# Optimization experiments

Hardware: AMD Instinct MI355X
Metric: run time of the kernel (lower is better)

Reference implementation:

```python
import jax, jax.numpy as jnp
import numpy as np

DIM = 256
N = 262144
LN_EPS = 1e-5


def setup_inputs() -> dict:
    key = jax.random.key(0)
    ks = jax.random.split(key, 16)
    d = DIM
    inp = {
        "x": jax.random.normal(ks[0], (N, d), dtype=jnp.float32),
        # main cell params (torch Linear stores weight as [out, in])
        "W_slow": jax.random.normal(ks[1], (d, d), dtype=jnp.float32) / np.sqrt(d),
        "V_slow": jax.random.normal(ks[2], (d, d), dtype=jnp.float32) * (0.1 / np.sqrt(d)),
        "gate_w": jax.random.normal(ks[3], (1, d), dtype=jnp.float32) / np.sqrt(d),
        "gate_b": jnp.zeros((1,), dtype=jnp.float32),
        # homeostatic core: Linear(4,16) -> LN(16) -> Tanh -> Linear(16,8) -> ReLU -> Linear(8,4) -> Sigmoid
        "sens1_w": jax.random.normal(ks[4], (16, 4), dtype=jnp.float32) * 0.5,
        "sens1_b": jnp.zeros((16,), dtype=jnp.float32),
        "ln_g": jnp.ones((16,), dtype=jnp.float32),
        "ln_b": jnp.zeros((16,), dtype=jnp.float32),
        "sens2_w": jax.random.normal(ks[5], (8, 16), dtype=jnp.float32) * 0.25,
        "sens2_b": jnp.zeros((8,), dtype=jnp.float32),
        "act_w": jax.random.normal(ks[6], (4, 8), dtype=jnp.float32) * 0.35,
        "act_b": jnp.zeros((4,), dtype=jnp.float32),
        # persistent Hebbian memory buffer
        "semantic_memory": jax.random.normal(ks[7], (d, d), dtype=jnp.float32) * 0.01,
    }
    return inp


def _homeostatic_controls(x, h_raw, w_norm, sens1_w, sens1_b, ln_g, ln_b,
                          sens2_w, sens2_b, act_w, act_b):
    # state vector: [surprise, excitation, fatigue, coherence]  -> [N, 4]
    surprise = jnp.abs(jnp.var(x, axis=1) - 0.5)          # unbiased=False variance
    excitation = jnp.mean(jnp.abs(h_raw), axis=1)
    fatigue = jnp.full_like(surprise, w_norm)
    coherence = jnp.full_like(surprise, 0.5)              # loss_val is None
    state = jnp.stack([surprise, excitation, fatigue, coherence], axis=1)
    z = state @ sens1_w.T + sens1_b                        # [N,16]
    mu = jnp.mean(z, axis=-1, keepdims=True)
    var = jnp.mean((z - mu) ** 2, axis=-1, keepdims=True)
    z = (z - mu) * jax.lax.rsqrt(var + LN_EPS) * ln_g + ln_b
    z = jnp.tanh(z)
    z = jax.nn.relu(z @ sens2_w.T + sens2_b)               # [N,8]
    controls = jax.nn.sigmoid(z @ act_w.T + act_b)         # [N,4]
    return controls


def reference(x, W_slow, V_slow, gate_w, gate_b,
              sens1_w, sens1_b, ln_g, ln_b, sens2_w, sens2_b, act_w, act_b,
              semantic_memory):
    # v = clamp(V_slow(x), -2, 2)
    v = jnp.clip(x @ V_slow.T, -2.0, 2.0)                  # [N, d]

    # homeostatic core (no_grad in torch)
    h_raw = x @ W_slow.T
    w_norm = jnp.linalg.norm(W_slow)
    controls = _homeostatic_controls(x, h_raw, w_norm, sens1_w, sens1_b,
                                     ln_g, ln_b, sens2_w, sens2_b, act_w, act_b)
    metabolic_rate = jnp.mean(controls[:, 0])
    gate_value = jnp.mean(controls[:, 2])

    gate = jax.nn.sigmoid(v @ gate_w.T + gate_b) * gate_value  # [N,1]
    output = jnp.clip(gate * v, -2.0, 2.0)

    # training-mode Hebbian memory update (no_grad in torch)
    batch = x.shape[0]
    hebb = (v.T @ x) / batch                               # [d, d]
    forget = jnp.mean(v ** 2, axis=0)[:, None] * semantic_memory
    delta = jnp.tanh(hebb - forget)
    mem = semantic_memory + delta * metabolic_rate * 0.1
    mem_norm = jnp.maximum(jnp.linalg.norm(mem), 1e-6)
    new_memory = mem / mem_norm * 0.5

    return output, new_memory
```

## Files before the change

kernel.cpp:

```cpp
#include <hip/hip_runtime.h>
#include <hip/hip_bf16.h>


#define NTOK 262144

typedef short s16x4 __attribute__((ext_vector_type(4)));
typedef short s16x8 __attribute__((ext_vector_type(8)));
typedef float f32x4 __attribute__((ext_vector_type(4)));
typedef unsigned int u32x4 __attribute__((ext_vector_type(4)));
typedef __bf16 bf16x8 __attribute__((ext_vector_type(8)));

static __device__ __forceinline__ float b2f(short s) {
  unsigned int u = ((unsigned int)(unsigned short)s) << 16;
  return __builtin_bit_cast(float, u);
}
static __device__ __forceinline__ short f2b(float f) {
  __hip_bfloat16 h = __float2bfloat16(f);
  return (short)__builtin_bit_cast(unsigned short, h);
}
static __device__ __forceinline__ float clip2(float f) {
  return fminf(2.f, fmaxf(-2.f, f));
}
static __device__ __forceinline__ unsigned int packu(short lo, short hi) {
  return (unsigned int)(unsigned short)lo | ((unsigned int)(unsigned short)hi << 16);
}
static __device__ __forceinline__ f32x4 mfma16(s16x8 a, s16x8 b, f32x4 c) {
  return __builtin_amdgcn_mfma_f32_16x16x32_bf16(
      __builtin_bit_cast(bf16x8, a), __builtin_bit_cast(bf16x8, b), c, 0, 0, 0);
}

__global__ __launch_bounds__(1024) void k_prep(const float* __restrict__ V,
                                               const float* __restrict__ W,
                                               short* __restrict__ Vb,
                                               short* __restrict__ Wb,
                                               float* __restrict__ scal) {
  int t = blockIdx.x * 1024 + threadIdx.x;
  f32x4 v4 = *(const f32x4*)(V + (size_t)t * 4);
  f32x4 w4 = *(const f32x4*)(W + (size_t)t * 4);
  s16x4 vb, wb;
  float s = 0.f;
#pragma unroll
  for (int e = 0; e < 4; ++e) {
    vb[e] = f2b(v4[e]);
    wb[e] = f2b(w4[e]);
    s += w4[e] * w4[e];
  }
  *(s16x4*)(Vb + (size_t)t * 4) = vb;
  *(s16x4*)(Wb + (size_t)t * 4) = wb;
#pragma unroll
  for (int d = 1; d < 64; d <<= 1) s += __shfl_xor(s, d);
  __shared__ float r[16];
  if ((threadIdx.x & 63) == 0) r[threadIdx.x >> 6] = s;
  __syncthreads();
  if (threadIdx.x == 0) {
    float tt = 0.f;
#pragma unroll
    for (int i = 0; i < 16; ++i) tt += r[i];
    atomicAdd(&scal[0], tt);
  }
}

__global__ __launch_bounds__(512) void k_main(
    const float* __restrict__ x, const short* __restrict__ Vb,
    const short* __restrict__ Wb, const float* __restrict__ gw,
    const float* __restrict__ gb, const float* __restrict__ s1w,
    const float* __restrict__ s1b, const float* __restrict__ lng,
    const float* __restrict__ lnb, const float* __restrict__ s2w,
    const float* __restrict__ s2b, const float* __restrict__ aw,
    const float* __restrict__ ab, short* __restrict__ v_out,
    float* __restrict__ g_out, float* __restrict__ scal) {
  __shared__ __align__(16) short xs[64 * 40];
  __shared__ float red[256];
  int tid = threadIdx.x;
  int lane = tid & 63, wid = tid >> 6;
  int lr = lane & 15, lg = lane >> 4;
  int mat = wid >> 2, wc = wid & 3;
  size_t r0 = (size_t)blockIdx.x * 64;

  f32x4 acc[4][4] = {};
  float sx = 0.f, sxx = 0.f;
  int srow = tid >> 3, skc = tid & 7;

  const short* Bm = mat ? Wb : Vb;
  const short* bbase = Bm + (size_t)(wc * 64 + lr) * 256 + lg * 8;
  const float* xsrc = x + (r0 + srow) * 256 + skc * 4;

  f32x4 rx = *(const f32x4*)(xsrc);
  s16x8 bcur[4], bnext[4];
#pragma unroll
  for (int nf = 0; nf < 4; ++nf)
    bcur[nf] = *(const s16x8*)(bbase + nf * 16 * 256);

#pragma unroll
  for (int ks = 0; ks < 8; ++ks) {
    {
      s16x4 c;
#pragma unroll
      for (int e = 0; e < 4; ++e) {
        float f = rx[e];
        sx += f;
        sxx += f * f;
        c[e] = f2b(f);
      }
      *(s16x4*)(xs + srow * 40 + skc * 4) = c;
    }
    __syncthreads();
    if (ks < 7) {
      rx = *(const f32x4*)(xsrc + (ks + 1) * 32);
#pragma unroll
      for (int nf = 0; nf < 4; ++nf)
        bnext[nf] = *(const s16x8*)(bbase + nf * 16 * 256 + (ks + 1) * 32);
    }
#pragma unroll
    for (int mf = 0; mf < 4; ++mf) {
      s16x8 a = *(const s16x8*)(xs + (mf * 16 + lr) * 40 + lg * 8);
#pragma unroll
      for (int nf = 0; nf < 4; ++nf)
        acc[mf][nf] = mfma16(a, bcur[nf], acc[mf][nf]);
    }
    __syncthreads();
#pragma unroll
    for (int nf = 0; nf < 4; ++nf) bcur[nf] = bnext[nf];
  }

  float pl[4][4];
  if (mat == 0) {
    float gw4[4];
#pragma unroll
    for (int nf = 0; nf < 4; ++nf) gw4[nf] = gw[wc * 64 + nf * 16 + lr];
#pragma unroll
    for (int mf = 0; mf < 4; ++mf)
#pragma unroll
      for (int e = 0; e < 4; ++e) {
        float g = 0.f;
#pragma unroll
        for (int nf = 0; nf < 4; ++nf) {
          float v = clip2(acc[mf][nf][e]);
          acc[mf][nf][e] = v;
          g += v * gw4[nf];
        }
        pl[mf][e] = g;
      }
  } else {
#pragma unroll
    for (int mf = 0; mf < 4; ++mf)
#pragma unroll
      for (int e = 0; e < 4; ++e) {
        float hbs = 0.f;
#pragma unroll
        for (int nf = 0; nf < 4; ++nf) hbs += fabsf(acc[mf][nf][e]);
        pl[mf][e] = hbs;
      }
  }
#pragma unroll
  for (int d = 1; d < 16; d <<= 1)
#pragma unroll
    for (int mf = 0; mf < 4; ++mf)
#pragma unroll
      for (int e = 0; e < 4; ++e) pl[mf][e] += __shfl_xor(pl[mf][e], d);
  sx += __shfl_xor(sx, 1); sx += __shfl_xor(sx, 2); sx += __shfl_xor(sx, 4);
  sxx += __shfl_xor(sxx, 1); sxx += __shfl_xor(sxx, 2); sxx += __shfl_xor(sxx, 4);

  if (tid < 128) red[tid] = 0.f;
  __syncthreads();
  if (lr == 0) {
#pragma unroll
    for (int mf = 0; mf < 4; ++mf)
#pragma unroll
      for (int e = 0; e < 4; ++e) {
        int row = mf * 16 + lg * 4 + e;
        atomicAdd(&red[mat * 64 + row], pl[mf][e]);
      }
  }
  if ((tid & 7) == 0) { red[128 + srow] = sx; red[192 + srow] = sxx; }
  if (mat == 0) {
#pragma unroll
    for (int mf = 0; mf < 4; ++mf)
#pragma unroll
      for (int nf = 0; nf < 4; ++nf)
#pragma unroll
        for (int e = 0; e < 4; ++e) {
          int row = mf * 16 + lg * 4 + e;
          int col = wc * 64 + nf * 16 + lr;
          v_out[(r0 + row) * 256 + col] = f2b(acc[mf][nf][e]);
        }
  }
  __syncthreads();

  float c0v = 0.f, c2v = 0.f;
  if (tid < 64) {
    int row = tid;
    float mean = red[128 + row] * (1.f / 256.f);
    float var = red[192 + row] * (1.f / 256.f) - mean * mean;
    float st[4];
    st[0] = fabsf(var - 0.5f);
    st[1] = red[64 + row] * (1.f / 256.f);
    st[2] = sqrtf(scal[0]);
    st[3] = 0.5f;
    float z[16];
#pragma unroll
    for (int o = 0; o < 16; ++o) {
      float a = s1b[o];
#pragma unroll
      for (int i = 0; i < 4; ++i) a += s1w[o * 4 + i] * st[i];
      z[o] = a;
    }
    float mu = 0.f;
#pragma unroll
    for (int o = 0; o < 16; ++o) mu += z[o];
    mu *= (1.f / 16.f);
    float vz = 0.f;
#pragma unroll
    for (int o = 0; o < 16; ++o) { float d2 = z[o] - mu; vz += d2 * d2; }
    vz *= (1.f / 16.f);
    float rs = rsqrtf(vz + 1e-5f);
#pragma unroll
    for (int o = 0; o < 16; ++o)
      z[o] = tanhf((z[o] - mu) * rs * lng[o] + lnb[o]);
    float z2[8];
#pragma unroll
    for (int o = 0; o < 8; ++o) {
      float a = s2b[o];
#pragma unroll
      for (int i = 0; i < 16; ++i) a += s2w[o * 16 + i] * z[i];
      z2[o] = fmaxf(a, 0.f);
    }
    float cc[2];
#pragma unroll
    for (int q = 0; q < 2; ++q) {
      int o = q * 2;
      float a = ab[o];
#pragma unroll
      for (int i = 0; i < 8; ++i) a += aw[o * 8 + i] * z2[i];
      cc[q] = 1.f / (1.f + expf(-a));
    }
    c0v = cc[0]; c2v = cc[1];
    float graw = red[row] + gb[0];
    g_out[r0 + row] = 1.f / (1.f + expf(-graw));
  }
#pragma unroll
  for (int d = 1; d < 64; d <<= 1) {
    c0v += __shfl_xor(c0v, d);
    c2v += __shfl_xor(c2v, d);
  }
  if (tid == 0) {
    atomicAdd(&scal[1], c0v);
    atomicAdd(&scal[2], c2v);
  }
}

__global__ __launch_bounds__(512, 2) void k_hebb(
    const float* __restrict__ x, const short* __restrict__ v_in,
    const float* __restrict__ g_sig, const float* __restrict__ scal,
    float* __restrict__ colv2, float* __restrict__ parts,
    float* __restrict__ out0) {
  __shared__ __align__(16) unsigned int ldsT[2 * 256 * 17];
  unsigned int* vT = ldsT;
  unsigned int* xT = ldsT + 256 * 17;
  int tid = threadIdx.x;
  int lane = tid & 63, wid = tid >> 6;
  int lr = lane & 15, lg = lane >> 4;
  int wr = wid >> 2, wc = wid & 3;
  size_t n0 = (size_t)blockIdx.x * 1024;
  float gv = scal[2] * (1.f / 262144.f);

  f32x4 acc[8][4] = {};
  float cv2[8] = {0.f, 0.f, 0.f, 0.f, 0.f, 0.f, 0.f, 0.f};
  int np = tid >> 5, ic = tid & 31, i0 = ic * 8;

  for (int nt = 0; nt < 32; ++nt) {
    size_t nr = n0 + nt * 32 + np * 2;
    s16x8 va = *(const s16x8*)(v_in + nr * 256 + i0);
    s16x8 vb = *(const s16x8*)(v_in + (nr + 1) * 256 + i0);
    f32x4 xa0 = *(const f32x4*)(x + nr * 256 + i0);
    f32x4 xa1 = *(const f32x4*)(x + nr * 256 + i0 + 4);
    f32x4 xb0 = *(const f32x4*)(x + (nr + 1) * 256 + i0);
    f32x4 xb1 = *(const f32x4*)(x + (nr + 1) * 256 + i0 + 4);
    float sa = g_sig[nr] * gv, sb = g_sig[nr + 1] * gv;
    f32x4 oa0, oa1, ob0, ob1;
#pragma unroll
    for (int j = 0; j < 4; ++j) {
      float fa = b2f(va[j]), fA = b2f(va[4 + j]);
      float fb = b2f(vb[j]), fB = b2f(vb[4 + j]);
      cv2[j] += fa * fa + fb * fb;
      cv2[4 + j] += fA * fA + fB * fB;
      oa0[j] = clip2(fa * sa); oa1[j] = clip2(fA * sa);
      ob0[j] = clip2(fb * sb); ob1[j] = clip2(fB * sb);
      vT[(i0 + j) * 17 + np] = packu(va[j], vb[j]);
      vT[(i0 + 4 + j) * 17 + np] = packu(va[4 + j], vb[4 + j]);
      xT[(i0 + j) * 17 + np] = packu(f2b(xa0[j]), f2b(xb0[j]));
      xT[(i0 + 4 + j) * 17 + np] = packu(f2b(xa1[j]), f2b(xb1[j]));
    }
    *(f32x4*)(out0 + nr * 256 + i0) = oa0;
    *(f32x4*)(out0 + nr * 256 + i0 + 4) = oa1;
    *(f32x4*)(out0 + (nr + 1) * 256 + i0) = ob0;
    *(f32x4*)(out0 + (nr + 1) * 256 + i0 + 4) = ob1;
    __syncthreads();
    int npb = lg * 4;
    s16x8 bfr[4];
#pragma unroll
    for (int nf = 0; nf < 4; ++nf) {
      int j = wc * 64 + nf * 16 + lr;
      u32x4 q;
      q[0] = xT[j * 17 + npb]; q[1] = xT[j * 17 + npb + 1];
      q[2] = xT[j * 17 + npb + 2]; q[3] = xT[j * 17 + npb + 3];
      bfr[nf] = __builtin_bit_cast(s16x8, q);
    }
#pragma unroll
    for (int mf = 0; mf < 8; ++mf) {
      int i = wr * 128 + mf * 16 + lr;
      u32x4 q;
      q[0] = vT[i * 17 + npb]; q[1] = vT[i * 17 + npb + 1];
      q[2] = vT[i * 17 + npb + 2]; q[3] = vT[i * 17 + npb + 3];
      s16x8 afr = __builtin_bit_cast(s16x8, q);
#pragma unroll
      for (int nf = 0; nf < 4; ++nf)
        acc[mf][nf] = mfma16(afr, bfr[nf], acc[mf][nf]);
    }
    __syncthreads();
  }
  float* myp = parts + (size_t)blockIdx.x * 65536;
#pragma unroll
  for (int mf = 0; mf < 8; ++mf)
#pragma unroll
    for (int nf = 0; nf < 4; ++nf)
#pragma unroll
      for (int e = 0; e < 4; ++e) {
        int i = wr * 128 + mf * 16 + lg * 4 + e;
        int j = wc * 64 + nf * 16 + lr;
        myp[i * 256 + j] = acc[mf][nf][e];
      }
  __syncthreads();
  float* cred = (float*)ldsT;
  if (tid < 256) cred[tid] = 0.f;
  __syncthreads();
#pragma unroll
  for (int j = 0; j < 8; ++j) atomicAdd(&cred[i0 + j], cv2[j]);
  __syncthreads();
  if (tid < 256) atomicAdd(&colv2[tid], cred[tid]);
}

__global__ __launch_bounds__(256) void k_mem1(
    const float* __restrict__ parts, const float* __restrict__ colv2,
    const float* __restrict__ sm, float* __restrict__ mem,
    float* __restrict__ scal) {
  int i = blockIdx.x, j = threadIdx.x;
  float hebb = 0.f;
#pragma unroll 8
  for (int p = 0; p < 256; ++p) hebb += parts[(size_t)p * 65536 + i * 256 + j];
  hebb *= (1.f / 262144.f);
  float mr = scal[1] * (1.f / 262144.f);
  float smv = sm[i * 256 + j];
  float forget = colv2[i] * (1.f / 262144.f) * smv;
  float delta = tanhf(hebb - forget);
  float m = smv + delta * mr * 0.1f;
  mem[i * 256 + j] = m;
  float s = m * m;
#pragma unroll
  for (int d = 1; d < 64; d <<= 1) s += __shfl_xor(s, d);
  __shared__ float r4[4];
  if ((j & 63) == 0) r4[j >> 6] = s;
  __syncthreads();
  if (j == 0) atomicAdd(&scal[3], r4[0] + r4[1] + r4[2] + r4[3]);
}

__global__ __launch_bounds__(256) void k_mem2(const float* __restrict__ mem,
                                              const float* __restrict__ scal,
                                              float* __restrict__ out1) {
  int idx = blockIdx.x * 256 + threadIdx.x;
  float scale = 0.5f / fmaxf(sqrtf(scal[3]), 1e-6f);
  out1[idx] = mem[idx] * scale;
}

extern "C" void kernel_launch(void* const* d_in, const int* in_sizes, int n_in,
                              void* d_out, int out_size, void* d_ws, size_t ws_size,
                              hipStream_t stream) {
  (void)in_sizes; (void)n_in; (void)out_size; (void)ws_size;
  const float* x   = (const float*)d_in[0];
  const float* Wm  = (const float*)d_in[1];
  const float* Vm  = (const float*)d_in[2];
  const float* gw  = (const float*)d_in[3];
  const float* gb  = (const float*)d_in[4];
  const float* s1w = (const float*)d_in[5];
  const float* s1b = (const float*)d_in[6];
  const float* lng = (const float*)d_in[7];
  const float* lnb = (const float*)d_in[8];
  const float* s2w = (const float*)d_in[9];
  const float* s2b = (const float*)d_in[10];
  const float* aw  = (const float*)d_in[11];
  const float* ab  = (const float*)d_in[12];
  const float* sm  = (const float*)d_in[13];
  float* out0 = (float*)d_out;
  float* out1 = out0 + (size_t)NTOK * 256;

  char* w = (char*)d_ws;
  short* v_ws  = (short*)w;
  float* g_ws  = (float*)(w + 134217728);
  float* scal  = (float*)(w + 135266304);
  float* colv2 = (float*)(w + 135266560);
  float* mem   = (float*)(w + 135267584);
  float* parts = (float*)(w + 135529728);
  short* Vb    = (short*)(w + 202638592);
  short* Wb    = (short*)(w + 202769664);

  hipMemsetAsync(scal, 0, 1280, stream);
  k_prep<<<16, 1024, 0, stream>>>(Vm, Wm, Vb, Wb, scal);
  k_main<<<4096, 512, 0, stream>>>(x, Vb, Wb, gw, gb, s1w, s1b, lng, lnb,
                                   s2w, s2b, aw, ab, v_ws, g_ws, scal);
  k_hebb<<<256, 512, 0, stream>>>(x, v_ws, g_ws, scal, colv2, parts, out0);
  k_mem1<<<256, 256, 0, stream>>>(parts, colv2, sm, mem, scal);
  k_mem2<<<256, 256, 0, stream>>>(mem, scal, out1);
}
```

Baseline: 408.8 us.

## Process four row tiles per block with double-buffered K=64 LDS pipeline in k_main

k_main now handles 256 rows per block (four 64-row tiles) instead of 64, and launches a quarter as many blocks. The K loop moves from K=32 steps to K=64 steps. It uses a double-buffered LDS tile with x loads issued two steps ahead, which leaves a single barrier per step. This is meant to hide global-load latency and amortise per-block setup. The cost is more registers, fewer blocks in flight, and a per-tile epilogue that is serialised inside each block.

```diff
diff --git a/kernel.cpp b/kernel.cpp
--- a/kernel.cpp
+++ b/kernel.cpp
@@ -69,184 +69,217 @@
     const float* __restrict__ s2b, const float* __restrict__ aw,
     const float* __restrict__ ab, short* __restrict__ v_out,
     float* __restrict__ g_out, float* __restrict__ scal) {
-  __shared__ __align__(16) short xs[64 * 40];
+  __shared__ __align__(16) short xs[2][64 * 72];
   __shared__ float red[256];
   int tid = threadIdx.x;
   int lane = tid & 63, wid = tid >> 6;
   int lr = lane & 15, lg = lane >> 4;
   int mat = wid >> 2, wc = wid & 3;
-  size_t r0 = (size_t)blockIdx.x * 64;
+  size_t bid = blockIdx.x;
 
   f32x4 acc[4][4] = {};
-  float sx = 0.f, sxx = 0.f;
+  float sx = 0.f, sxx = 0.f, sx_t = 0.f, sxx_t = 0.f;
   int srow = tid >> 3, skc = tid & 7;
 
   const short* Bm = mat ? Wb : Vb;
   const short* bbase = Bm + (size_t)(wc * 64 + lr) * 256 + lg * 8;
-  const float* xsrc = x + (r0 + srow) * 256 + skc * 4;
-
-  f32x4 rx = *(const f32x4*)(xsrc);
-  s16x8 bcur[4], bnext[4];
-#pragma unroll
-  for (int nf = 0; nf < 4; ++nf)
-    bcur[nf] = *(const s16x8*)(bbase + nf * 16 * 256);
-
-#pragma unroll
-  for (int ks = 0; ks < 8; ++ks) {
-    {
-      s16x4 c;
-#pragma unroll
-      for (int e = 0; e < 4; ++e) {
-        float f = rx[e];
-        sx += f;
-        sxx += f * f;
-        c[e] = f2b(f);
-      }
-      *(s16x4*)(xs + srow * 40 + skc * 4) = c;
-    }
+
+  f32x4 rxa0, rxb0, rxa1, rxb1;
+
+#define XPTR(c)                                                         \
+  (x + ((size_t)bid * 256 + (size_t)((c) >> 2) * 64 + srow) * 256 +     \
+   ((c) & 3) * 64 + skc * 8)
+#define ISSUE(c, A, B_)                      \
+  {                                          \
+    int cc = (c) > 15 ? 15 : (c);            \
+    const float* p_ = XPTR(cc);              \
+    A = *(const f32x4*)p_;                   \
+    B_ = *(const f32x4*)(p_ + 4);            \
+  }
+#define CONVERT(A, B_, buf)                                   \
+  {                                                           \
+    s16x8 c8;                                                 \
+    _Pragma("unroll") for (int e = 0; e < 4; ++e) {           \
+      float f0 = A[e], f1 = B_[e];                            \
+      sx += f0 + f1;                                          \
+      sxx += f0 * f0 + f1 * f1;                               \
+      c8[e] = f2b(f0);                                        \
+      c8[4 + e] = f2b(f1);                                    \
+    }                                                         \
+    *(s16x8*)(&xs[buf][srow * 72 + skc * 8]) = c8;            \
+  }
+#define STEP(g, RAi, RBi, RAc, RBc)                                        \
+  {                                                                        \
+    ISSUE((g) + 2, RAi, RBi);                                              \
+    s16x8 bfr[4][2];                                                       \
+    _Pragma("unroll") for (int nf = 0; nf < 4; ++nf)                       \
+        _Pragma("unroll") for (int kk = 0; kk < 2; ++kk)                   \
+            bfr[nf][kk] = *(const s16x8*)(bbase + nf * 16 * 256 +          \
+                                          ((g) & 3) * 64 + kk * 32);       \
+    CONVERT(RAc, RBc, ((g) + 1) & 1);                                      \
+    _Pragma("unroll") for (int mf = 0; mf < 4; ++mf) {                     \
+      s16x8 a0 = *(const s16x8*)(&xs[(g) & 1][(mf * 16 + lr) * 72 +        \
+                                              lg * 8]);                    \
+      s16x8 a1 = *(const s16x8*)(&xs[(g) & 1][(mf * 16 + lr) * 72 + 32 +   \
+                                              lg * 8]);                    \
+      _Pragma("unroll") for (int nf = 0; nf < 4; ++nf) {                   \
+        acc[mf][nf] = mfma16(a0, bfr[nf][0], acc[mf][nf]);                 \
+        acc[mf][nf] = mfma16(a1, bfr[nf][1], acc[mf][nf]);                 \
+      }                                                                    \
+    }                                                                      \
+    __syncthreads();                                                       \
+  }
+
+  ISSUE(0, rxa0, rxb0);
+  ISSUE(1, rxa1, rxb1);
+  CONVERT(rxa0, rxb0, 0);
+  __syncthreads();
+
+  for (int t = 0; t < 4; ++t) {
+    int g0 = t * 4;
+    STEP(g0 + 0, rxa0, rxb0, rxa1, rxb1);
+    STEP(g0 + 1, rxa1, rxb1, rxa0, rxb0);
+    STEP(g0 + 2, rxa0, rxb0, rxa1, rxb1);
+    sx_t = sx; sxx_t = sxx; sx = 0.f; sxx = 0.f;
+    STEP(g0 + 3, rxa1, rxb1, rxa0, rxb0);
+
+    size_t r0 = bid * 256 + (size_t)t * 64;
+    float pl[4][4];
+    if (mat == 0) {
+      float gw4[4];
+#pragma unroll
+      for (int nf = 0; nf < 4; ++nf) gw4[nf] = gw[wc * 64 + nf * 16 + lr];
+#pragma unroll
+      for (int mf = 0; mf < 4; ++mf)
+#pragma unroll
+        for (int e = 0; e < 4; ++e) {
+          float g = 0.f;
+#pragma unroll
+          for (int nf = 0; nf < 4; ++nf) {
+            float v = clip2(acc[mf][nf][e]);
+            acc[mf][nf][e] = v;
+            g += v * gw4[nf];
+          }
+          pl[mf][e] = g;
+        }
+    } else {
+#pragma unroll
+      for (int mf = 0; mf < 4; ++mf)
+#pragma unroll
+        for (int e = 0; e < 4; ++e) {
+          float hbs = 0.f;
+#pragma unroll
+          for (int nf = 0; nf < 4; ++nf) hbs += fabsf(acc[mf][nf][e]);
+          pl[mf][e] = hbs;
+        }
+    }
+#pragma unroll
+    for (int d = 1; d < 16; d <<= 1)
+#pragma unroll
+      for (int mf = 0; mf < 4; ++mf)
+#pragma unroll
+        for (int e = 0; e < 4; ++e) pl[mf][e] += __shfl_xor(pl[mf][e], d);
+    sx_t += __shfl_xor(sx_t, 1); sx_t += __shfl_xor(sx_t, 2);
+    sx_t += __shfl_xor(sx_t, 4);
+    sxx_t += __shfl_xor(sxx_t, 1); sxx_t += __shfl_xor(sxx_t, 2);
+    sxx_t += __shfl_xor(sxx_t, 4);
+
+    if (tid < 128) red[tid] = 0.f;
     __syncthreads();
-    if (ks < 7) {
-      rx = *(const f32x4*)(xsrc + (ks + 1) * 32);
-#pragma unroll
-      for (int nf = 0; nf < 4; ++nf)
-        bnext[nf] = *(const s16x8*)(bbase + nf * 16 * 256 + (ks + 1) * 32);
-    }
-#pragma unroll
-    for (int mf = 0; mf < 4; ++mf) {
-      s16x8 a = *(const s16x8*)(xs + (mf * 16 + lr) * 40 + lg * 8);
-#pragma unroll
-      for (int nf = 0; nf < 4; ++nf)
-        acc[mf][nf] = mfma16(a, bcur[nf], acc[mf][nf]);
-    }
-    __syncthreads();
-#pragma unroll
-    for (int nf = 0; nf < 4; ++nf) bcur[nf] = bnext[nf];
-  }
-
-  float pl[4][4];
-  if (mat == 0) {
-    float gw4[4];
-#pragma unroll
-    for (int nf = 0; nf < 4; ++nf) gw4[nf] = gw[wc * 64 + nf * 16 + lr];
-#pragma unroll
-    for (int mf = 0; mf < 4; ++mf)
-#pragma unroll
-      for (int e = 0; e < 4; ++e) {
-        float g = 0.f;
-#pragma unroll
-        for (int nf = 0; nf < 4; ++nf) {
-          float v = clip2(acc[mf][nf][e]);
-          acc[mf][nf][e] = v;
-          g += v * gw4[nf];
-        }
-        pl[mf][e] = g;
-      }
-  } else {
-#pragma unroll
-    for (int mf = 0; mf < 4; ++mf)
-#pragma unroll
-      for (int e = 0; e < 4; ++e) {
-        float hbs = 0.f;
-#pragma unroll
-        for (int nf = 0; nf < 4; ++nf) hbs += fabsf(acc[mf][nf][e]);
-        pl[mf][e] = hbs;
-      }
-  }
-#pragma unroll
-  for (int d = 1; d < 16; d <<= 1)
-#pragma unroll
-    for (int mf = 0; mf < 4; ++mf)
-#pragma unroll
-      for (int e = 0; e < 4; ++e) pl[mf][e] += __shfl_xor(pl[mf][e], d);
-  sx += __shfl_xor(sx, 1); sx += __shfl_xor(sx, 2); sx += __shfl_xor(sx, 4);
-  sxx += __shfl_xor(sxx, 1); sxx += __shfl_xor(sxx, 2); sxx += __shfl_xor(sxx, 4);
-
-  if (tid < 128) red[tid] = 0.f;
-  __syncthreads();
-  if (lr == 0) {
-#pragma unroll
-    for (int mf = 0; mf < 4; ++mf)
-#pragma unroll
-      for (int e = 0; e < 4; ++e) {
-        int row = mf * 16 + lg * 4 + e;
-        atomicAdd(&red[mat * 64 + row], pl[mf][e]);
-      }
-  }
-  if ((tid & 7) == 0) { red[128 + srow] = sx; red[192 + srow] = sxx; }
-  if (mat == 0) {
-#pragma unroll
-    for (int mf = 0; mf < 4; ++mf)
-#pragma unroll
-      for (int nf = 0; nf < 4; ++nf)
+    if (lr == 0) {
+#pragma unroll
+      for (int mf = 0; mf < 4; ++mf)
 #pragma unroll
         for (int e = 0; e < 4; ++e) {
           int row = mf * 16 + lg * 4 + e;
-          int col = wc * 64 + nf * 16 + lr;
-          v_out[(r0 + row) * 256 + col] = f2b(acc[mf][nf][e]);
+          atomicAdd(&red[mat * 64 + row], pl[mf][e]);
         }
-  }
-  __syncthreads();
-
-  float c0v = 0.f, c2v = 0.f;
-  if (tid < 64) {
-    int row = tid;
-    float mean = red[128 + row] * (1.f / 256.f);
-    float var = red[192 + row] * (1.f / 256.f) - mean * mean;
-    float st[4];
-    st[0] = fabsf(var - 0.5f);
-    st[1] = red[64 + row] * (1.f / 256.f);
-    st[2] = sqrtf(scal[0]);
-    st[3] = 0.5f;
-    float z[16];
-#pragma unroll
-    for (int o = 0; o < 16; ++o) {
-      float a = s1b[o];
-#pragma unroll
-      for (int i = 0; i < 4; ++i) a += s1w[o * 4 + i] * st[i];
-      z[o] = a;
-    }
-    float mu = 0.f;
-#pragma unroll
-    for (int o = 0; o < 16; ++o) mu += z[o];
-    mu *= (1.f / 16.f);
-    float vz = 0.f;
-#pragma unroll
-    for (int o = 0; o < 16; ++o) { float d2 = z[o] - mu; vz += d2 * d2; }
-    vz *= (1.f / 16.f);
-    float rs = rsqrtf(vz + 1e-5f);
-#pragma unroll
-    for (int o = 0; o < 16; ++o)
-      z[o] = tanhf((z[o] - mu) * rs * lng[o] + lnb[o]);
-    float z2[8];
-#pragma unroll
-    for (int o = 0; o < 8; ++o) {
-      float a = s2b[o];
-#pragma unroll
-      for (int i = 0; i < 16; ++i) a += s2w[o * 16 + i] * z[i];
-      z2[o] = fmaxf(a, 0.f);
-    }
-    float cc[2];
-#pragma unroll
-    for (int q = 0; q < 2; ++q) {
-      int o = q * 2;
-      float a = ab[o];
-#pragma unroll
-      for (int i = 0; i < 8; ++i) a += aw[o * 8 + i] * z2[i];
-      cc[q] = 1.f / (1.f + expf(-a));
-    }
-    c0v = cc[0]; c2v = cc[1];
-    float graw = red[row] + gb[0];
-    g_out[r0 + row] = 1.f / (1.f + expf(-graw));
-  }
-#pragma unroll
-  for (int d = 1; d < 64; d <<= 1) {
-    c0v += __shfl_xor(c0v, d);
-    c2v += __shfl_xor(c2v, d);
-  }
-  if (tid == 0) {
-    atomicAdd(&scal[1], c0v);
-    atomicAdd(&scal[2], c2v);
-  }
+    }
+    if (skc == 0) { red[128 + srow] = sx_t; red[192 + srow] = sxx_t; }
+    if (mat == 0) {
+#pragma unroll
+      for (int mf = 0; mf < 4; ++mf)
+#pragma unroll
+        for (int nf = 0; nf < 4; ++nf)
+#pragma unroll
+          for (int e = 0; e < 4; ++e) {
+            int row = mf * 16 + lg * 4 + e;
+            int col = wc * 64 + nf * 16 + lr;
+            v_out[(r0 + row) * 256 + col] = f2b(acc[mf][nf][e]);
+          }
+    }
+    __syncthreads();
+
+    float c0v = 0.f, c2v = 0.f;
+    if (tid < 64) {
+      int row = tid;
+      float mean = red[128 + row] * (1.f / 256.f);
+      float var = red[192 + row] * (1.f / 256.f) - mean * mean;
+      float st[4];
+      st[0] = fabsf(var - 0.5f);
+      st[1] = red[64 + row] * (1.f / 256.f);
+      st[2] = sqrtf(scal[0]);
+      st[3] = 0.5f;
+      float z[16];
+#pragma unroll
+      for (int o = 0; o < 16; ++o) {
+        float a = s1b[o];
+#pragma unroll
+        for (int i = 0; i < 4; ++i) a += s1w[o * 4 + i] * st[i];
+        z[o] = a;
+      }
+      float mu = 0.f;
+#pragma unroll
+      for (int o = 0; o < 16; ++o) mu += z[o];
+      mu *= (1.f / 16.f);
+      float vz = 0.f;
+#pragma unroll
+      for (int o = 0; o < 16; ++o) { float d2 = z[o] - mu; vz += d2 * d2; }
+      vz *= (1.f / 16.f);
+      float rs = rsqrtf(vz + 1e-5f);
+#pragma unroll
+      for (int o = 0; o < 16; ++o)
+        z[o] = tanhf((z[o] - mu) * rs * lng[o] + lnb[o]);
+      float z2[8];
+#pragma unroll
+      for (int o = 0; o < 8; ++o) {
+        float a = s2b[o];
+#pragma unroll
+        for (int i = 0; i < 16; ++i) a += s2w[o * 16 + i] * z[i];
+        z2[o] = fmaxf(a, 0.f);
+      }
+      float cc[2];
+#pragma unroll
+      for (int q = 0; q < 2; ++q) {
+        int o = q * 2;
+        float a = ab[o];
+#pragma unroll
+        for (int i = 0; i < 8; ++i) a += aw[o * 8 + i] * z2[i];
+        cc[q] = 1.f / (1.f + expf(-a));
+      }
+      c0v = cc[0]; c2v = cc[1];
+      float graw = red[row] + gb[0];
+      g_out[r0 + row] = 1.f / (1.f + expf(-graw));
+    }
+#pragma unroll
+    for (int d = 1; d < 64; d <<= 1) {
+      c0v += __shfl_xor(c0v, d);
+      c2v += __shfl_xor(c2v, d);
+    }
+    if (tid == 0) {
+      atomicAdd(&scal[1], c0v);
+      atomicAdd(&scal[2], c2v);
+    }
+#pragma unroll
+    for (int mf = 0; mf < 4; ++mf)
+#pragma unroll
+      for (int nf = 0; nf < 4; ++nf)
+        acc[mf][nf] = (f32x4){0.f, 0.f, 0.f, 0.f};
+  }
+#undef STEP
+#undef CONVERT
+#undef ISSUE
+#undef XPTR
 }
 
 __global__ __launch_bounds__(512, 2) void k_hebb(
@@ -405,7 +438,7 @@
 
   hipMemsetAsync(scal, 0, 1280, stream);
   k_prep<<<16, 1024, 0, stream>>>(Vm, Wm, Vb, Wb, scal);
-  k_main<<<4096, 512, 0, stream>>>(x, Vb, Wb, gw, gb, s1w, s1b, lng, lnb,
+  k_main<<<1024, 512, 0, stream>>>(x, Vb, Wb, gw, gb, s1w, s1b, lng, lnb,
                                    s2w, s2b, aw, ab, v_ws, g_ws, scal);
   k_hebb<<<256, 512, 0, stream>>>(x, v_ws, g_ws, scal, colv2, parts, out0);
   k_mem1<<<256, 256, 0, stream>>>(parts, colv2, sm, mem, scal);
```

Result: slower. 475.8 us (+16.4%).

## Shrink k_main tile to 32 rows with 256-thread blocks and wider warp column spans

Applied to the files above, without the earlier changes.

Reorganizes the main GEMM kernel from 64-row, 8-wave blocks to 32-row, 4-wave blocks. Each wave now covers 128 output columns (8 fragments) for 2 row fragments instead of 4x4. The cross-iteration B register prefetch is dropped, with B fragments loaded inside the k-loop. The aim is more resident blocks and less register pressure (launch_bounds 256,3), at the cost of reading the weight matrices twice as often per row and losing the prefetch overlap.

```diff
diff --git a/kernel.cpp b/kernel.cpp
--- a/kernel.cpp
+++ b/kernel.cpp
@@ -60,7 +60,7 @@
   }
 }
 
-__global__ __launch_bounds__(512) void k_main(
+__global__ __launch_bounds__(256, 3) void k_main(
     const float* __restrict__ x, const short* __restrict__ Vb,
     const short* __restrict__ Wb, const float* __restrict__ gw,
     const float* __restrict__ gb, const float* __restrict__ s1w,
@@ -69,29 +69,24 @@
     const float* __restrict__ s2b, const float* __restrict__ aw,
     const float* __restrict__ ab, short* __restrict__ v_out,
     float* __restrict__ g_out, float* __restrict__ scal) {
-  __shared__ __align__(16) short xs[64 * 40];
-  __shared__ float red[256];
+  __shared__ __align__(16) short xs[32 * 40];
+  __shared__ float red[128];
   int tid = threadIdx.x;
   int lane = tid & 63, wid = tid >> 6;
   int lr = lane & 15, lg = lane >> 4;
-  int mat = wid >> 2, wc = wid & 3;
-  size_t r0 = (size_t)blockIdx.x * 64;
-
-  f32x4 acc[4][4] = {};
+  int mat = wid >> 1, half = wid & 1;
+  size_t r0 = (size_t)blockIdx.x * 32;
+
+  f32x4 acc[2][8] = {};
   float sx = 0.f, sxx = 0.f;
   int srow = tid >> 3, skc = tid & 7;
 
   const short* Bm = mat ? Wb : Vb;
-  const short* bbase = Bm + (size_t)(wc * 64 + lr) * 256 + lg * 8;
+  const short* bbase = Bm + (size_t)(half * 128 + lr) * 256 + lg * 8;
   const float* xsrc = x + (r0 + srow) * 256 + skc * 4;
 
   f32x4 rx = *(const f32x4*)(xsrc);
-  s16x8 bcur[4], bnext[4];
-#pragma unroll
-  for (int nf = 0; nf < 4; ++nf)
-    bcur[nf] = *(const s16x8*)(bbase + nf * 16 * 256);
-
-#pragma unroll
+
   for (int ks = 0; ks < 8; ++ks) {
     {
       s16x4 c;
@@ -105,96 +100,97 @@
       *(s16x4*)(xs + srow * 40 + skc * 4) = c;
     }
     __syncthreads();
-    if (ks < 7) {
-      rx = *(const f32x4*)(xsrc + (ks + 1) * 32);
-#pragma unroll
-      for (int nf = 0; nf < 4; ++nf)
-        bnext[nf] = *(const s16x8*)(bbase + nf * 16 * 256 + (ks + 1) * 32);
-    }
-#pragma unroll
-    for (int mf = 0; mf < 4; ++mf) {
-      s16x8 a = *(const s16x8*)(xs + (mf * 16 + lr) * 40 + lg * 8);
-#pragma unroll
-      for (int nf = 0; nf < 4; ++nf)
-        acc[mf][nf] = mfma16(a, bcur[nf], acc[mf][nf]);
+    if (ks < 7) rx = *(const f32x4*)(xsrc + (ks + 1) * 32);
+    int k0 = ks * 32;
+    s16x8 a0 = *(const s16x8*)(xs + lr * 40 + lg * 8);
+    s16x8 a1 = *(const s16x8*)(xs + (16 + lr) * 40 + lg * 8);
+#pragma unroll
+    for (int q = 0; q < 2; ++q) {
+      s16x8 bq[4];
+#pragma unroll
+      for (int j = 0; j < 4; ++j)
+        bq[j] = *(const s16x8*)(bbase + (q * 64 + j * 16) * 256 + k0);
+#pragma unroll
+      for (int j = 0; j < 4; ++j) {
+        acc[0][q * 4 + j] = mfma16(a0, bq[j], acc[0][q * 4 + j]);
+        acc[1][q * 4 + j] = mfma16(a1, bq[j], acc[1][q * 4 + j]);
+      }
     }
     __syncthreads();
-#pragma unroll
-    for (int nf = 0; nf < 4; ++nf) bcur[nf] = bnext[nf];
-  }
-
-  float pl[4][4];
+  }
+
+  float pl[2][4];
   if (mat == 0) {
-    float gw4[4];
-#pragma unroll
-    for (int nf = 0; nf < 4; ++nf) gw4[nf] = gw[wc * 64 + nf * 16 + lr];
-#pragma unroll
-    for (int mf = 0; mf < 4; ++mf)
+    float gw8[8];
+#pragma unroll
+    for (int nf = 0; nf < 8; ++nf) gw8[nf] = gw[half * 128 + nf * 16 + lr];
+#pragma unroll
+    for (int mf = 0; mf < 2; ++mf)
 #pragma unroll
       for (int e = 0; e < 4; ++e) {
         float g = 0.f;
 #pragma unroll
-        for (int nf = 0; nf < 4; ++nf) {
+        for (int nf = 0; nf < 8; ++nf) {
           float v = clip2(acc[mf][nf][e]);
           acc[mf][nf][e] = v;
-          g += v * gw4[nf];
+          g += v * gw8[nf];
         }
         pl[mf][e] = g;
       }
   } else {
 #pragma unroll
-    for (int mf = 0; mf < 4; ++mf)
+    for (int mf = 0; mf < 2; ++mf)
 #pragma unroll
       for (int e = 0; e < 4; ++e) {
         float hbs = 0.f;
 #pragma unroll
-        for (int nf = 0; nf < 4; ++nf) hbs += fabsf(acc[mf][nf][e]);
+        for (int nf = 0; nf < 8; ++nf) hbs += fabsf(acc[mf][nf][e]);
         pl[mf][e] = hbs;
       }
   }
 #pragma unroll
   for (int d = 1; d < 16; d <<= 1)
 #pragma unroll
-    for (int mf = 0; mf < 4; ++mf)
+    for (int mf = 0; mf < 2; ++mf)
 #pragma unroll
       for (int e = 0; e < 4; ++e) pl[mf][e] += __shfl_xor(pl[mf][e], d);
   sx += __shfl_xor(sx, 1); sx += __shfl_xor(sx, 2); sx += __shfl_xor(sx, 4);
   sxx += __shfl_xor(sxx, 1); sxx += __shfl_xor(sxx, 2); sxx += __shfl_xor(sxx, 4);
 
-  if (tid < 128) red[tid] = 0.f;
+  if (tid < 64) red[tid] = 0.f;
   __syncthreads();
   if (lr == 0) {
 #pragma unroll
-    for (int mf = 0; mf < 4; ++mf)
+    for (int mf = 0; mf < 2; ++mf)
 #pragma unroll
       for (int e = 0; e < 4; ++e) {
         int row = mf * 16 + lg * 4 + e;
-        atomicAdd(&red[mat * 64 + row], pl[mf][e]);
-      }
-  }
-  if ((tid & 7) == 0) { red[128 + srow] = sx; red[192 + srow] = sxx; }
+        atomicAdd(&red[mat * 32 + row], pl[mf][e]);
+      }
+  }
+  if (skc == 0) { red[64 + srow] = sx; red[96 + srow] = sxx; }
   if (mat == 0) {
 #pragma unroll
-    for (int mf = 0; mf < 4; ++mf)
-#pragma unroll
-      for (int nf = 0; nf < 4; ++nf)
+    for (int mf = 0; mf < 2; ++mf)
+#pragma unroll
+      for (int nf = 0; nf < 8; ++nf)
 #pragma unroll
         for (int e = 0; e < 4; ++e) {
           int row = mf * 16 + lg * 4 + e;
-          int col = wc * 64 + nf * 16 + lr;
+          int col = half * 128 + nf * 16 + lr;
           v_out[(r0 + row) * 256 + col] = f2b(acc[mf][nf][e]);
         }
   }
   __syncthreads();
 
   float c0v = 0.f, c2v = 0.f;
-  if (tid < 64) {
+  if (tid < 32) {
     int row = tid;
-    float mean = red[128 + row] * (1.f / 256.f);
-    float var = red[192 + row] * (1.f / 256.f) - mean * mean;
+    float mean = red[64 + row] * (1.f / 256.f);
+    float var = red[96 + row] * (1.f / 256.f) - mean * mean;
     float st[4];
     st[0] = fabsf(var - 0.5f);
-    st[1] = red[64 + row] * (1.f / 256.f);
+    st[1] = red[32 + row] * (1.f / 256.f);
     st[2] = sqrtf(scal[0]);
     st[3] = 0.5f;
     float z[16];
@@ -405,7 +401,7 @@
 
   hipMemsetAsync(scal, 0, 1280, stream);
   k_prep<<<16, 1024, 0, stream>>>(Vm, Wm, Vb, Wb, scal);
-  k_main<<<4096, 512, 0, stream>>>(x, Vb, Wb, gw, gb, s1w, s1b, lng, lnb,
+  k_main<<<8192, 256, 0, stream>>>(x, Vb, Wb, gw, gb, s1w, s1b, lng, lnb,
                                    s2w, s2b, aw, ab, v_ws, g_ws, scal);
   k_hebb<<<256, 512, 0, stream>>>(x, v_ws, g_ws, scal, colv2, parts, out0);
   k_mem1<<<256, 256, 0, stream>>>(parts, colv2, sm, mem, scal);
```

After: 499.6 us. 1.22x slower.
